# Optimization experiments

Measured on AMD Instinct MI355X. Metric: run time of the kernel, lower is better.

Reference implementation:

```python
import jax, jax.numpy as jnp
import numpy as np

B, L, SIZE, BACK, H = 4, 1024, 1024, 512, 16
D = SIZE // H  # head_size = 64


def setup_inputs() -> dict:
    key = jax.random.key(0)
    ks = jax.random.split(key, 18)
    s = 0.02
    return {
        "k": jax.random.normal(ks[0], (B, L, SIZE), jnp.float32),
        "v": jax.random.normal(ks[1], (B, L, SIZE), jnp.float32),
        "q": jax.random.normal(ks[2], (B, L, SIZE), jnp.float32),
        "background": jax.random.normal(ks[3], (B, L, BACK), jnp.float32),
        # weights stored [in, out] (pre-transposed vs torch Linear)
        "Wk": jax.random.normal(ks[4], (SIZE, SIZE), jnp.float32) * s,
        "bk": jnp.zeros((SIZE,), jnp.float32),
        "Wv": jax.random.normal(ks[5], (SIZE, SIZE), jnp.float32) * s,
        "bv": jnp.zeros((SIZE,), jnp.float32),
        "Wq": jax.random.normal(ks[6], (SIZE, SIZE), jnp.float32) * s,
        "bq": jnp.zeros((SIZE,), jnp.float32),
        "Wb": jax.random.normal(ks[7], (BACK, SIZE), jnp.float32) * s,
        "bb": jnp.zeros((SIZE,), jnp.float32),
        "Wo": jax.random.normal(ks[8], (SIZE, SIZE), jnp.float32) * s,
        "bo": jnp.zeros((SIZE,), jnp.float32),
    }


def _heads(x):
    # [B, L, H*D] -> [B, H, L, D]
    b, l, _ = x.shape
    return x.reshape(b, l, H, D).transpose(0, 2, 1, 3)


def reference(k, v, q, background, Wk, bk, Wv, bv, Wq, bq, Wb, bb, Wo, bo):
    kh = _heads(k @ Wk + bk)
    vh = _heads(v @ Wv + bv)
    qh = _heads(q @ Wq + bq) / jnp.sqrt(jnp.asarray(D, k.dtype))
    gh = _heads(background @ Wb + bb)
    scores = jnp.einsum("bhqd,bhkd->bhqk", qh, kh)   # [B,H,Lq,Lk]
    gates = jax.nn.sigmoid(jnp.einsum("bhqd,bhkd->bhqk", qh, gh))
    attn = jax.nn.softmax(scores, axis=-1) * gates    # dropout = identity (eval)
    ctx = jnp.einsum("bhqk,bhkd->bhqd", attn, vh)
    ctx = ctx.transpose(0, 2, 1, 3).reshape(k.shape[0], -1, H * D)
    return ctx @ Wo + bo
```

## Files before the change

kernel.cpp:

```cpp
#include <hip/hip_runtime.h>
#include <cstddef>
#include <cstdint>

typedef __attribute__((ext_vector_type(8))) short s16x8;
typedef __attribute__((ext_vector_type(4))) short s16x4;
typedef __attribute__((ext_vector_type(4))) float f32x4;

#define MFMA(a, b, c) __builtin_amdgcn_mfma_f32_16x16x32_bf16(a, b, c, 0, 0, 0)
#define LOG2E 1.44269504088896f

__device__ __forceinline__ short f2bf(float x) {
    uint32_t u = __float_as_uint(x);
    u = (u + 0x7FFFu + ((u >> 16) & 1u)) >> 16;
    return (short)u;
}

__device__ __forceinline__ void gld16(const void* g, void* l) {
    __builtin_amdgcn_global_load_lds(
        (const __attribute__((address_space(1))) unsigned int*)g,
        (__attribute__((address_space(3))) unsigned int*)l, 16, 0, 0);
}

__device__ __forceinline__ float fexp2(float x) {
#if __has_builtin(__builtin_amdgcn_exp2f)
    return __builtin_amdgcn_exp2f(x);
#else
    return exp2f(x);
#endif
}

__device__ __forceinline__ float frcp(float x) {
#if __has_builtin(__builtin_amdgcn_rcpf)
    return __builtin_amdgcn_rcpf(x);
#else
    return 1.f / x;
#endif
}

__device__ __forceinline__ unsigned cvtpk(float lo, float hi) {
    unsigned r;
    asm("v_cvt_pk_bf16_f32 %0, %1, %2" : "=v"(r) : "v"(lo), "v"(hi));
    return r;
}

struct ConvP { const float* in[4]; short* out[4]; };

__global__ __launch_bounds__(256)
void conv_all(ConvP p) {
    const int i = blockIdx.x * 256 + threadIdx.x;
    int r, base;
    if (i < 524288)            { r = 0; base = 0; }
    else if (i < 1048576)      { r = 1; base = 524288; }
    else if (i < 1310720)      { r = 2; base = 1048576; }
    else                       { r = 3; base = 1310720; }
    const int j = i - base;
    const float4 a = *(const float4*)(p.in[r] + (size_t)j * 8);
    const float4 b = *(const float4*)(p.in[r] + (size_t)j * 8 + 4);
    s16x8 o;
    o[0] = f2bf(a.x); o[1] = f2bf(a.y); o[2] = f2bf(a.z); o[3] = f2bf(a.w);
    o[4] = f2bf(b.x); o[5] = f2bf(b.y); o[6] = f2bf(b.z); o[7] = f2bf(b.w);
    *(s16x8*)(p.out[r] + (size_t)j * 8) = o;
}

struct WtP { const float* W[5]; short* Wt[5]; int K[5]; };

__global__ __launch_bounds__(256)
void conv_wt_b(WtP p) {
    __shared__ float T[64][65];
    const int z = blockIdx.z;
    const int K = p.K[z];
    const int k0 = blockIdx.y << 6, n0 = blockIdx.x << 6;
    if (k0 >= K) return;
    const float* W = p.W[z];
    short* Wt = p.Wt[z];
    const int tr = threadIdx.x >> 4, tc4 = (threadIdx.x & 15) << 2;
    #pragma unroll
    for (int i = 0; i < 4; ++i) {
        const int r = tr + i * 16;
        const float4 v = *(const float4*)(W + (size_t)(k0 + r) * 1024 + n0 + tc4);
        T[r][tc4 + 0] = v.x; T[r][tc4 + 1] = v.y;
        T[r][tc4 + 2] = v.z; T[r][tc4 + 3] = v.w;
    }
    __syncthreads();
    #pragma unroll
    for (int i = 0; i < 4; ++i) {
        const int nr = tr + i * 16;
        s16x4 o;
        o[0] = f2bf(T[tc4 + 0][nr]); o[1] = f2bf(T[tc4 + 1][nr]);
        o[2] = f2bf(T[tc4 + 2][nr]); o[3] = f2bf(T[tc4 + 3][nr]);
        *(s16x4*)(Wt + (size_t)(n0 + nr) * K + k0 + tc4) = o;
    }
}

struct Proj5P {
    const short* A[5]; const short* Bt[5]; const float* bias[5];
    void* Y[5]; int Kd[5]; float alpha[5]; int mode[5];
};

__global__ __launch_bounds__(256, 2)
void proj_gemm128d(Proj5P p, int zbase) {
    __shared__ __align__(16) short lds[2 * 16384];

    const int tid = threadIdx.x;
    const int w = tid >> 6, lane = tid & 63;
    const int la = lane & 15, kg = lane >> 4;
    const int wr = w >> 1, wc = w & 1;

    const int cpx = gridDim.x >> 3;
    const int orig = blockIdx.x;
    const int swz = (orig & 7) * cpx + (orig >> 3);
    const int z = zbase + (swz >> 8);
    const int rem = swz & 255;
    const int bm = rem >> 3, bn = rem & 7;

    const short* __restrict__ A  = p.A[z];
    const short* __restrict__ Bt = p.Bt[z];
    const int K = p.Kd[z];
    const int NT = K >> 6;

    const int srow = tid >> 3;
    const int csrc = (tid & 7) ^ (srow & 7);
    const short* gA = A  + (size_t)(bm * 128 + srow) * K + csrc * 8;
    const short* gB = Bt + (size_t)(bn * 128 + srow) * K + csrc * 8;
    short* dstA = &lds[srow * 64 + (tid & 7) * 8];
    short* dstB = dstA + 8192;

#define STAGE(t, nb) do {                                                  \
        const size_t ko_ = (size_t)((t) << 6);                             \
        short* ba_ = dstA + (nb) * 16384;                                  \
        short* bb_ = dstB + (nb) * 16384;                                  \
        _Pragma("unroll")                                                  \
        for (int i = 0; i < 4; ++i) {                                      \
            gld16(gA + (size_t)(32 * i) * K + ko_, ba_ + i * 2048);        \
            gld16(gB + (size_t)(32 * i) * K + ko_, bb_ + i * 2048);       \
        }                                                                  \
    } while (0)

    const int c0 = kg ^ (la & 7), c1 = (4 + kg) ^ (la & 7);
    const int aRd = (wr * 64 + la) * 64;
    const int bRd = 8192 + (wc * 64 + la) * 64;

    f32x4 acc[4][4] = {};

    STAGE(0, 0);
    asm volatile("s_waitcnt vmcnt(0)" ::: "memory");
    asm volatile("s_barrier" ::: "memory");

    for (int t = 0; t < NT; ++t) {
        const int cb = (t & 1) * 16384;
        if (t + 1 < NT) STAGE(t + 1, (t & 1) ^ 1);
        s16x8 af[4][2], bf[4][2];
        #pragma unroll
        for (int m = 0; m < 4; ++m) {
            af[m][0] = *(const s16x8*)&lds[cb + aRd + m * 1024 + c0 * 8];
            af[m][1] = *(const s16x8*)&lds[cb + aRd + m * 1024 + c1 * 8];
        }
        #pragma unroll
        for (int n = 0; n < 4; ++n) {
            bf[n][0] = *(const s16x8*)&lds[cb + bRd + n * 1024 + c0 * 8];
            bf[n][1] = *(const s16x8*)&lds[cb + bRd + n * 1024 + c1 * 8];
        }
        __builtin_amdgcn_s_setprio(1);
        #pragma unroll
        for (int m = 0; m < 4; ++m)
            #pragma unroll
            for (int n = 0; n < 4; ++n) {
                acc[m][n] = MFMA(af[m][0], bf[n][0], acc[m][n]);
                acc[m][n] = MFMA(af[m][1], bf[n][1], acc[m][n]);
            }
        __builtin_amdgcn_s_setprio(0);
        if (t + 1 < NT) {
            asm volatile("s_waitcnt vmcnt(0)" ::: "memory");
            asm volatile("s_barrier" ::: "memory");
        }
    }
#undef STAGE

    const float* __restrict__ bias = p.bias[z];
    const float alpha = p.alpha[z];
    const int mode = p.mode[z];

    if (mode == 2) {
        short* __restrict__ Y = (short*)p.Y[z];
        short* Tv = lds;
        asm volatile("s_waitcnt lgkmcnt(0)" ::: "memory");
        asm volatile("s_barrier" ::: "memory");
        #pragma unroll
        for (int ni = 0; ni < 4; ++ni) {
            const int rrow = wc * 64 + ni * 16 + la;
            const float bs = bias[bn * 128 + rrow];
            #pragma unroll
            for (int mi = 0; mi < 4; ++mi) {
                const int l0 = wr * 64 + mi * 16 + kg * 4;
                const unsigned d0 = cvtpk(alpha * (acc[mi][ni][0] + bs),
                                          alpha * (acc[mi][ni][1] + bs));
                const unsigned d1 = cvtpk(alpha * (acc[mi][ni][2] + bs),
                                          alpha * (acc[mi][ni][3] + bs));
                *(unsigned*)&Tv[rrow * 132 + l0]     = d0;
                *(unsigned*)&Tv[rrow * 132 + l0 + 2] = d1;
            }
        }
        asm volatile("s_barrier" ::: "memory");
        const int bb_ = (bm * 128) >> 10;
        const int l0g = (bm * 128) & 1023;
        #pragma unroll
        for (int s = 0; s < 8; ++s) {
            const int c = tid + (s << 8);
            const int rr = c >> 4, seg = c & 15;
            const int hh = bn * 2 + (rr >> 6), dd = rr & 63;
            const s16x8 vv = *(const s16x8*)&Tv[rr * 132 + seg * 8];
            *(s16x8*)&Y[((((size_t)bb_ * 16 + hh) * 64 + dd) << 10) + l0g + seg * 8] = vv;
        }
        return;
    }

    #pragma unroll
    for (int n = 0; n < 4; ++n) {
        const int col = bn * 128 + wc * 64 + n * 16 + la;
        const float bs = bias[col];
        #pragma unroll
        for (int m = 0; m < 4; ++m) {
            const int row0 = bm * 128 + wr * 64 + m * 16 + kg * 4;
            #pragma unroll
            for (int r = 0; r < 4; ++r) {
                const float v = alpha * (acc[m][n][r] + bs);
                if (mode == 0) {
                    ((short*)p.Y[z])[(size_t)(row0 + r) * 1024 + col] = f2bf(v);
                } else {
                    ((float*)p.Y[z])[(size_t)(row0 + r) * 1024 + col] = v;
                }
            }
        }
    }
}

__global__ __launch_bounds__(512)
void attn_mfma(const short* __restrict__ qh, const short* __restrict__ kh,
               const short* __restrict__ gh, const short* __restrict__ vt,
               short* __restrict__ ctx) {
    __shared__ __align__(16) short lds[33792];

    const int tid = threadIdx.x, w = tid >> 6, lane = tid & 63;
    const int la = lane & 15, kg = lane >> 4;

    const int orig = blockIdx.x;
    const int xcd = orig & 7, i = orig >> 3;
    const int bh = xcd * 8 + (i >> 3);
    const int qt = i & 7;
    const int b = bh >> 4, h = bh & 15;
    const int q0 = qt << 7;

    const size_t hb = ((size_t)b << 20) + ((size_t)h << 6);
    const size_t vtbase = ((size_t)bh) << 16;

    const int qrow = q0 + w * 16 + la;
    const s16x8 aq0 = *(const s16x8*)(qh + hb + (size_t)qrow * 1024 + kg * 8);
    const s16x8 aq1 = *(const s16x8*)(qh + hb + (size_t)qrow * 1024 + 32 + kg * 8);

    const int sr = tid >> 3, sc = tid & 7;
    const int cs = sc ^ (sr & 7);
    const short* ksrc = kh + hb + (size_t)sr * 1024 + cs * 8;
    const short* gsrc = gh + hb + (size_t)sr * 1024 + cs * 8;
    const short* vsrc = vt + vtbase + (size_t)sr * 1024 + cs * 8;
    const int sdst = tid * 8;

    const int ch0 = (kg ^ (la & 7)) * 8;
    const int ch1 = ((4 + kg) ^ (la & 7)) * 8;
    const int pbase = 24576 + w * 1152;

    float s_run = 0.f;
    f32x4 o[4] = {};

#define ASTG(kt, bb) do {                                                  \
        const size_t kr_ = (size_t)((kt) << 6) * 1024;                     \
        gld16(ksrc + kr_, &lds[(bb) * 4096 + sdst]);                       \
        gld16(gsrc + kr_, &lds[8192 + (bb) * 4096 + sdst]);                \
        gld16(vsrc + ((kt) << 6), &lds[16384 + (bb) * 4096 + sdst]);       \
    } while (0)

    ASTG(0, 0);
    asm volatile("s_waitcnt vmcnt(0)" ::: "memory");
    asm volatile("s_barrier" ::: "memory");

    for (int kt = 0; kt < 16; ++kt) {
        const int cb = (kt & 1) * 4096;
        if (kt < 15) ASTG(kt + 1, (kt + 1) & 1);

        f32x4 st[4] = {}, gt[4] = {};
        #pragma unroll
        for (int nf = 0; nf < 4; ++nf) {
            const int rb = cb + (nf * 16 + la) * 64;
            const s16x8 kb0 = *(const s16x8*)&lds[rb + ch0];
            const s16x8 kb1 = *(const s16x8*)&lds[rb + ch1];
            st[nf] = MFMA(kb0, aq0, st[nf]);
            st[nf] = MFMA(kb1, aq1, st[nf]);
            const s16x8 gb0 = *(const s16x8*)&lds[8192 + rb + ch0];
            const s16x8 gb1 = *(const s16x8*)&lds[8192 + rb + ch1];
            gt[nf] = MFMA(gb0, aq0, gt[nf]);
            gt[nf] = MFMA(gb1, aq1, gt[nf]);
        }

        float ps = 0.f;
        unsigned pkw[4][2];
        #pragma unroll
        for (int nf = 0; nf < 4; ++nf) {
            const float p0 = fexp2(st[nf][0]);
            const float p1 = fexp2(st[nf][1]);
            const float p2 = fexp2(st[nf][2]);
            const float p3 = fexp2(st[nf][3]);
            ps += (p0 + p1) + (p2 + p3);
            const float g0 = frcp(1.f + fexp2(-gt[nf][0]));
            const float g1 = frcp(1.f + fexp2(-gt[nf][1]));
            const float g2 = frcp(1.f + fexp2(-gt[nf][2]));
            const float g3 = frcp(1.f + fexp2(-gt[nf][3]));
            pkw[nf][0] = cvtpk(p0 * g0, p1 * g1);
            pkw[nf][1] = cvtpk(p2 * g2, p3 * g3);
        }
        s_run += ps;

        #pragma unroll
        for (int nf = 0; nf < 4; ++nf) {
            *(unsigned*)&lds[pbase + la * 72 + nf * 16 + kg * 4]     = pkw[nf][0];
            *(unsigned*)&lds[pbase + la * 72 + nf * 16 + kg * 4 + 2] = pkw[nf][1];
        }

        const s16x8 pa0 = *(const s16x8*)&lds[pbase + la * 72 + kg * 8];
        const s16x8 pa1 = *(const s16x8*)&lds[pbase + la * 72 + 32 + kg * 8];
        #pragma unroll
        for (int nf = 0; nf < 4; ++nf) {
            const int rb = cb + (nf * 16 + la) * 64;
            const s16x8 vb0 = *(const s16x8*)&lds[16384 + rb + ch0];
            const s16x8 vb1 = *(const s16x8*)&lds[16384 + rb + ch1];
            o[nf] = MFMA(vb0, pa0, o[nf]);
            o[nf] = MFMA(vb1, pa1, o[nf]);
        }

        if (kt < 15) {
            asm volatile("s_waitcnt vmcnt(0)" ::: "memory");
            asm volatile("s_barrier" ::: "memory");
        }
    }
#undef ASTG

    float sv = s_run;
    sv += __shfl_xor(sv, 16);
    sv += __shfl_xor(sv, 32);
    const float inv = frcp(sv);
    short* crow = ctx + ((size_t)(b * 1024 + qrow) << 10) + (h << 6);
    #pragma unroll
    for (int nf = 0; nf < 4; ++nf) {
        *(unsigned*)(crow + nf * 16 + kg * 4)     = cvtpk(o[nf][0] * inv, o[nf][1] * inv);
        *(unsigned*)(crow + nf * 16 + kg * 4 + 2) = cvtpk(o[nf][2] * inv, o[nf][3] * inv);
    }
}

extern "C" void kernel_launch(void* const* d_in, const int* in_sizes, int n_in,
                              void* d_out, int out_size, void* d_ws, size_t ws_size,
                              hipStream_t stream) {
    (void)in_sizes; (void)n_in; (void)out_size; (void)ws_size;

    const float* k  = (const float*)d_in[0];
    const float* v  = (const float*)d_in[1];
    const float* q  = (const float*)d_in[2];
    const float* bg = (const float*)d_in[3];
    const float* Wk = (const float*)d_in[4];  const float* bk = (const float*)d_in[5];
    const float* Wv = (const float*)d_in[6];  const float* bv = (const float*)d_in[7];
    const float* Wq = (const float*)d_in[8];  const float* bq = (const float*)d_in[9];
    const float* Wb = (const float*)d_in[10]; const float* bb = (const float*)d_in[11];
    const float* Wo = (const float*)d_in[12]; const float* bo = (const float*)d_in[13];

    short* ws = (short*)d_ws;
    const size_t MN = (size_t)4096 * 1024;
    short* khb = ws;
    short* qhb = ws + MN;
    short* ghb = ws + 2 * MN;
    short* vtb = ws + 3 * MN;
    short* xk  = ws + 4 * MN;
    short* xq  = ws + 5 * MN;
    short* xg  = ws + 6 * MN;
    short* xv  = ws + 6 * MN + MN / 2;
    short* wkt = ws + 7 * MN + MN / 2;
    short* wvt = wkt + 1048576;
    short* wqt = wvt + 1048576;
    short* wot = wqt + 1048576;
    short* wbt = wot + 1048576;
    short* ctxb = xk;

    const dim3 blk(256);

    WtP wp;
    wp.W[0] = Wk; wp.Wt[0] = wkt; wp.K[0] = 1024;
    wp.W[1] = Wv; wp.Wt[1] = wvt; wp.K[1] = 1024;
    wp.W[2] = Wq; wp.Wt[2] = wqt; wp.K[2] = 1024;
    wp.W[3] = Wb; wp.Wt[3] = wbt; wp.K[3] = 512;
    wp.W[4] = Wo; wp.Wt[4] = wot; wp.K[4] = 1024;
    conv_wt_b<<<dim3(16, 16, 5), blk, 0, stream>>>(wp);

    ConvP cp;
    cp.in[0] = k;  cp.out[0] = xk;
    cp.in[1] = q;  cp.out[1] = xq;
    cp.in[2] = bg; cp.out[2] = xg;
    cp.in[3] = v;  cp.out[3] = xv;
    conv_all<<<7168, blk, 0, stream>>>(cp);

    Proj5P p5;
    p5.A[0] = xk;   p5.Bt[0] = wkt; p5.bias[0] = bk; p5.Y[0] = khb;
    p5.Kd[0] = 1024; p5.alpha[0] = LOG2E;  p5.mode[0] = 0;
    p5.A[1] = xq;   p5.Bt[1] = wqt; p5.bias[1] = bq; p5.Y[1] = qhb;
    p5.Kd[1] = 1024; p5.alpha[1] = 0.125f; p5.mode[1] = 0;
    p5.A[2] = xg;   p5.Bt[2] = wbt; p5.bias[2] = bb; p5.Y[2] = ghb;
    p5.Kd[2] = 512;  p5.alpha[2] = LOG2E;  p5.mode[2] = 0;
    p5.A[3] = xv;   p5.Bt[3] = wvt; p5.bias[3] = bv; p5.Y[3] = vtb;
    p5.Kd[3] = 1024; p5.alpha[3] = 1.0f;   p5.mode[3] = 2;
    p5.A[4] = ctxb; p5.Bt[4] = wot; p5.bias[4] = bo; p5.Y[4] = d_out;
    p5.Kd[4] = 1024; p5.alpha[4] = 1.0f;   p5.mode[4] = 1;

    proj_gemm128d<<<dim3(1024), blk, 0, stream>>>(p5, 0);

    attn_mfma<<<dim3(512), dim3(512), 0, stream>>>(qhb, khb, ghb, vtb, ctxb);

    proj_gemm128d<<<dim3(256), blk, 0, stream>>>(p5, 4);
}
```

Before: 118.6 us.

## Use 256x256 ping-pong GEMM for QKVG projections and 128x64 tiles for output

The four input projections move to a new 512-thread kernel with 256x256 tiles. It splits each K-step into 32-wide halves, interleaves LDS reads, async global-to-LDS loads and MFMA phases across barriers, and launches exactly 256 blocks, one per CU. The output projection gets a dedicated kernel with 128x64 tiles and 512 blocks so that more blocks cover the CUs. Attention MFMA sections also get setprio hints. The larger tiles raise arithmetic intensity at the cost of a single block per CU and tighter barrier-driven scheduling.

```diff
diff --git a/kernel.cpp b/kernel.cpp
--- a/kernel.cpp
+++ b/kernel.cpp
@@ -92,71 +92,234 @@
     }
 }
 
-struct Proj5P {
-    const short* A[5]; const short* Bt[5]; const float* bias[5];
-    void* Y[5]; int Kd[5]; float alpha[5]; int mode[5];
+struct Proj4P {
+    const short* A[4]; const short* Bt[4]; const float* bias[4];
+    short* Y[4]; int Kd[4]; float alpha[4]; int mode[4];
 };
 
-__global__ __launch_bounds__(256, 2)
-void proj_gemm128d(Proj5P p, int zbase) {
-    __shared__ __align__(16) short lds[2 * 16384];
+__global__ __launch_bounds__(512, 1)
+void proj_gemm256p(Proj4P p) {
+    __shared__ __align__(16) short lds[65536];
+
+    const int tid = threadIdx.x;
+    const int w = tid >> 6, lane = tid & 63;
+    const int la = lane & 15, kg = lane >> 4;
+    const int wr = w >> 2, wc = w & 3;
+
+    const int orig = blockIdx.x;
+    const int swz = (orig & 7) * 32 + (orig >> 3);
+    const int z = swz >> 6;
+    const int rem = swz & 63;
+    const int bm = rem >> 2, bn = rem & 3;
+
+    const short* __restrict__ A  = p.A[z];
+    const short* __restrict__ Bt = p.Bt[z];
+    const int K = p.Kd[z];
+    const int NT = K >> 6;
+
+    const int sr = tid >> 2, sc = tid & 3;
+    const int csw = sc ^ ((sr >> 1) & 3);
+    const short* gA = A  + (size_t)(bm * 256 + sr) * K + csw * 8;
+    const short* gB = Bt + (size_t)(bn * 256 + sr) * K + csw * 8;
+    const int sdst = sr * 32 + sc * 8;
+
+#define STG_A(kt, buf, ks) do {                                            \
+        const size_t off_ = (size_t)((kt) * 64 + (ks) * 32);               \
+        short* d_ = &lds[(buf) * 16384 + (ks) * 8192 + sdst];              \
+        gld16(gA + off_, d_);                                              \
+        gld16(gA + (size_t)128 * K + off_, d_ + 4096);                     \
+    } while (0)
+#define STG_B(kt, buf, ks) do {                                            \
+        const size_t off_ = (size_t)((kt) * 64 + (ks) * 32);               \
+        short* d_ = &lds[32768 + (buf) * 16384 + (ks) * 8192 + sdst];      \
+        gld16(gB + off_, d_);                                              \
+        gld16(gB + (size_t)128 * K + off_, d_ + 4096);                     \
+    } while (0)
+
+    const int ach = (kg ^ ((la >> 1) & 3)) * 8;
+    const int aRow = (wr * 128 + la) * 32;
+    const int bRow = 32768 + (wc * 64 + la) * 32;
+
+    s16x8 af[4], bf[4];
+    f32x4 acc[8][4] = {};
+
+#define LDA(buf, mh, ks) do { _Pragma("unroll")                            \
+    for (int mf = 0; mf < 4; ++mf)                                         \
+        af[mf] = *(const s16x8*)&lds[(buf) * 16384 + (ks) * 8192 + aRow    \
+                                     + (mh) * 2048 + mf * 512 + ach];      \
+    } while (0)
+#define LDB(buf, ks) do { _Pragma("unroll")                                \
+    for (int nf = 0; nf < 4; ++nf)                                         \
+        bf[nf] = *(const s16x8*)&lds[(buf) * 16384 + (ks) * 8192 + bRow    \
+                                     + nf * 512 + ach];                    \
+    } while (0)
+#define MF(mh) do { __builtin_amdgcn_s_setprio(1); _Pragma("unroll")       \
+    for (int mf = 0; mf < 4; ++mf) _Pragma("unroll")                       \
+    for (int nf = 0; nf < 4; ++nf)                                         \
+        acc[(mh) * 4 + mf][nf] = MFMA(af[mf], bf[nf], acc[(mh) * 4 + mf][nf]); \
+    __builtin_amdgcn_s_setprio(0); } while (0)
+#define BARR() __builtin_amdgcn_s_barrier()
+#define LGKM0() do { asm volatile("s_waitcnt lgkmcnt(0)" ::: "memory");    \
+                     __builtin_amdgcn_sched_barrier(0); } while (0)
+#define VMW(n) asm volatile("s_waitcnt vmcnt(" #n ")" ::: "memory")
+
+    STG_A(0, 0, 0); STG_B(0, 0, 0);
+    STG_A(0, 0, 1); STG_B(0, 0, 1);
+    STG_A(1, 1, 0); STG_B(1, 1, 0);
+    VMW(8);
+    BARR();
+
+    for (int t = 0; t < NT; ++t) {
+        const int buf = t & 1, nbuf = buf ^ 1;
+        LDA(buf, 0, 0); LDB(buf, 0);
+        if (t + 1 < NT) STG_A(t + 1, nbuf, 1);
+        BARR(); LGKM0(); MF(0);
+        BARR();
+        LDA(buf, 1, 0);
+        if (t + 1 < NT) STG_B(t + 1, nbuf, 1);
+        BARR(); LGKM0(); MF(1);
+        if (t + 1 < NT) { VMW(6); } else { VMW(0); }
+        BARR();
+        LDA(buf, 1, 1); LDB(buf, 1);
+        if (t + 2 < NT) STG_A(t + 2, buf, 0);
+        BARR(); LGKM0(); MF(1);
+        BARR();
+        LDA(buf, 0, 1);
+        if (t + 2 < NT) STG_B(t + 2, buf, 0);
+        BARR(); LGKM0(); MF(0);
+        if (t + 2 < NT) { VMW(6); } else if (t + 1 < NT) { VMW(2); }
+        BARR();
+    }
+#undef STG_A
+#undef STG_B
+#undef LDA
+#undef LDB
+#undef MF
+
+    const float* __restrict__ bias = p.bias[z];
+    const float alpha = p.alpha[z];
+
+    if (p.mode[z] == 0) {
+        short* __restrict__ Y = p.Y[z];
+        #pragma unroll
+        for (int nf = 0; nf < 4; ++nf) {
+            const int col = bn * 256 + wc * 64 + nf * 16 + la;
+            const float bs = bias[col];
+            #pragma unroll
+            for (int g = 0; g < 8; ++g) {
+                const int row0 = bm * 256 + wr * 128 + (g >> 2) * 64 + (g & 3) * 16 + kg * 4;
+                #pragma unroll
+                for (int r = 0; r < 4; ++r)
+                    Y[(size_t)(row0 + r) * 1024 + col] = f2bf(alpha * (acc[g][nf][r] + bs));
+            }
+        }
+        return;
+    }
+
+    {
+        short* __restrict__ Y = p.Y[z];
+        const int bb_ = (bm * 256) >> 10;
+        const int l0g = (bm * 256) & 1023;
+        #pragma unroll
+        for (int ph = 0; ph < 2; ++ph) {
+            BARR();
+            if ((wc >> 1) == ph) {
+                #pragma unroll
+                for (int nf = 0; nf < 4; ++nf) {
+                    const int col = wc * 64 + nf * 16 + la;
+                    const int cp = col - ph * 128;
+                    const float bs = bias[bn * 256 + col];
+                    #pragma unroll
+                    for (int g = 0; g < 8; ++g) {
+                        const int row = wr * 128 + (g >> 2) * 64 + (g & 3) * 16 + kg * 4;
+                        const unsigned d0 = cvtpk(alpha * (acc[g][nf][0] + bs),
+                                                  alpha * (acc[g][nf][1] + bs));
+                        const unsigned d1 = cvtpk(alpha * (acc[g][nf][2] + bs),
+                                                  alpha * (acc[g][nf][3] + bs));
+                        *(unsigned*)&lds[cp * 264 + row]     = d0;
+                        *(unsigned*)&lds[cp * 264 + row + 2] = d1;
+                    }
+                }
+            }
+            asm volatile("s_waitcnt lgkmcnt(0)" ::: "memory");
+            BARR();
+            const int cp = tid >> 2;
+            const int colg = bn * 256 + ph * 128 + cp;
+            const int hh = colg >> 6, dd = colg & 63;
+            const size_t ybase = ((((size_t)bb_ * 16 + hh) * 64 + dd) << 10) + l0g;
+            #pragma unroll
+            for (int s = 0; s < 8; ++s) {
+                const int rchunk = (tid & 3) + s * 4;
+                *(s16x8*)&Y[ybase + rchunk * 8] =
+                    *(const s16x8*)&lds[cp * 264 + rchunk * 8];
+            }
+            BARR();
+        }
+    }
+#undef BARR
+#undef LGKM0
+#undef VMW
+}
+
+struct ProjOP {
+    const short* A; const short* Bt; const float* bias; float* Y;
+};
+
+__global__ __launch_bounds__(256, 3)
+void proj_gemmO(ProjOP p) {
+    __shared__ __align__(16) short lds[2 * 12288];
 
     const int tid = threadIdx.x;
     const int w = tid >> 6, lane = tid & 63;
     const int la = lane & 15, kg = lane >> 4;
     const int wr = w >> 1, wc = w & 1;
 
-    const int cpx = gridDim.x >> 3;
     const int orig = blockIdx.x;
-    const int swz = (orig & 7) * cpx + (orig >> 3);
-    const int z = zbase + (swz >> 8);
-    const int rem = swz & 255;
-    const int bm = rem >> 3, bn = rem & 7;
-
-    const short* __restrict__ A  = p.A[z];
-    const short* __restrict__ Bt = p.Bt[z];
-    const int K = p.Kd[z];
-    const int NT = K >> 6;
+    const int swz = (orig & 7) * 64 + (orig >> 3);
+    const int bm = swz >> 4, bn = swz & 15;
+
+    const int K = 1024, NT = 16;
 
     const int srow = tid >> 3;
     const int csrc = (tid & 7) ^ (srow & 7);
-    const short* gA = A  + (size_t)(bm * 128 + srow) * K + csrc * 8;
-    const short* gB = Bt + (size_t)(bn * 128 + srow) * K + csrc * 8;
+    const short* gA = p.A  + (size_t)(bm * 128 + srow) * K + csrc * 8;
+    const short* gB = p.Bt + (size_t)(bn * 64 + srow) * K + csrc * 8;
     short* dstA = &lds[srow * 64 + (tid & 7) * 8];
     short* dstB = dstA + 8192;
 
 #define STAGE(t, nb) do {                                                  \
         const size_t ko_ = (size_t)((t) << 6);                             \
-        short* ba_ = dstA + (nb) * 16384;                                  \
-        short* bb_ = dstB + (nb) * 16384;                                  \
         _Pragma("unroll")                                                  \
-        for (int i = 0; i < 4; ++i) {                                      \
-            gld16(gA + (size_t)(32 * i) * K + ko_, ba_ + i * 2048);        \
-            gld16(gB + (size_t)(32 * i) * K + ko_, bb_ + i * 2048);       \
-        }                                                                  \
+        for (int i = 0; i < 4; ++i)                                        \
+            gld16(gA + (size_t)(32 * i) * K + ko_,                         \
+                  dstA + (nb) * 12288 + i * 2048);                         \
+        _Pragma("unroll")                                                  \
+        for (int i = 0; i < 2; ++i)                                        \
+            gld16(gB + (size_t)(32 * i) * K + ko_,                         \
+                  dstB + (nb) * 12288 + i * 2048);                         \
     } while (0)
 
     const int c0 = kg ^ (la & 7), c1 = (4 + kg) ^ (la & 7);
     const int aRd = (wr * 64 + la) * 64;
-    const int bRd = 8192 + (wc * 64 + la) * 64;
-
-    f32x4 acc[4][4] = {};
+    const int bRd = 8192 + (wc * 32 + la) * 64;
+
+    f32x4 acc[4][2] = {};
 
     STAGE(0, 0);
     asm volatile("s_waitcnt vmcnt(0)" ::: "memory");
     asm volatile("s_barrier" ::: "memory");
 
     for (int t = 0; t < NT; ++t) {
-        const int cb = (t & 1) * 16384;
+        const int cb = (t & 1) * 12288;
         if (t + 1 < NT) STAGE(t + 1, (t & 1) ^ 1);
-        s16x8 af[4][2], bf[4][2];
+        s16x8 af[4][2], bf[2][2];
         #pragma unroll
         for (int m = 0; m < 4; ++m) {
             af[m][0] = *(const s16x8*)&lds[cb + aRd + m * 1024 + c0 * 8];
             af[m][1] = *(const s16x8*)&lds[cb + aRd + m * 1024 + c1 * 8];
         }
         #pragma unroll
-        for (int n = 0; n < 4; ++n) {
+        for (int n = 0; n < 2; ++n) {
             bf[n][0] = *(const s16x8*)&lds[cb + bRd + n * 1024 + c0 * 8];
             bf[n][1] = *(const s16x8*)&lds[cb + bRd + n * 1024 + c1 * 8];
         }
@@ -164,7 +327,7 @@
         #pragma unroll
         for (int m = 0; m < 4; ++m)
             #pragma unroll
-            for (int n = 0; n < 4; ++n) {
+            for (int n = 0; n < 2; ++n) {
                 acc[m][n] = MFMA(af[m][0], bf[n][0], acc[m][n]);
                 acc[m][n] = MFMA(af[m][1], bf[n][1], acc[m][n]);
             }
@@ -176,60 +339,16 @@
     }
 #undef STAGE
 
-    const float* __restrict__ bias = p.bias[z];
-    const float alpha = p.alpha[z];
-    const int mode = p.mode[z];
-
-    if (mode == 2) {
-        short* __restrict__ Y = (short*)p.Y[z];
-        short* Tv = lds;
-        asm volatile("s_waitcnt lgkmcnt(0)" ::: "memory");
-        asm volatile("s_barrier" ::: "memory");
-        #pragma unroll
-        for (int ni = 0; ni < 4; ++ni) {
-            const int rrow = wc * 64 + ni * 16 + la;
-            const float bs = bias[bn * 128 + rrow];
-            #pragma unroll
-            for (int mi = 0; mi < 4; ++mi) {
-                const int l0 = wr * 64 + mi * 16 + kg * 4;
-                const unsigned d0 = cvtpk(alpha * (acc[mi][ni][0] + bs),
-                                          alpha * (acc[mi][ni][1] + bs));
-                const unsigned d1 = cvtpk(alpha * (acc[mi][ni][2] + bs),
-                                          alpha * (acc[mi][ni][3] + bs));
-                *(unsigned*)&Tv[rrow * 132 + l0]     = d0;
-                *(unsigned*)&Tv[rrow * 132 + l0 + 2] = d1;
-            }
-        }
-        asm volatile("s_barrier" ::: "memory");
-        const int bb_ = (bm * 128) >> 10;
-        const int l0g = (bm * 128) & 1023;
-        #pragma unroll
-        for (int s = 0; s < 8; ++s) {
-            const int c = tid + (s << 8);
-            const int rr = c >> 4, seg = c & 15;
-            const int hh = bn * 2 + (rr >> 6), dd = rr & 63;
-            const s16x8 vv = *(const s16x8*)&Tv[rr * 132 + seg * 8];
-            *(s16x8*)&Y[((((size_t)bb_ * 16 + hh) * 64 + dd) << 10) + l0g + seg * 8] = vv;
-        }
-        return;
-    }
-
     #pragma unroll
-    for (int n = 0; n < 4; ++n) {
-        const int col = bn * 128 + wc * 64 + n * 16 + la;
-        const float bs = bias[col];
+    for (int n = 0; n < 2; ++n) {
+        const int col = bn * 64 + wc * 32 + n * 16 + la;
+        const float bs = p.bias[col];
         #pragma unroll
         for (int m = 0; m < 4; ++m) {
             const int row0 = bm * 128 + wr * 64 + m * 16 + kg * 4;
             #pragma unroll
-            for (int r = 0; r < 4; ++r) {
-                const float v = alpha * (acc[m][n][r] + bs);
-                if (mode == 0) {
-                    ((short*)p.Y[z])[(size_t)(row0 + r) * 1024 + col] = f2bf(v);
-                } else {
-                    ((float*)p.Y[z])[(size_t)(row0 + r) * 1024 + col] = v;
-                }
-            }
+            for (int r = 0; r < 4; ++r)
+                p.Y[(size_t)(row0 + r) * 1024 + col] = acc[m][n][r] + bs;
         }
     }
 }
@@ -287,6 +406,7 @@
         if (kt < 15) ASTG(kt + 1, (kt + 1) & 1);
 
         f32x4 st[4] = {}, gt[4] = {};
+        __builtin_amdgcn_s_setprio(1);
         #pragma unroll
         for (int nf = 0; nf < 4; ++nf) {
             const int rb = cb + (nf * 16 + la) * 64;
@@ -299,6 +419,7 @@
             gt[nf] = MFMA(gb0, aq0, gt[nf]);
             gt[nf] = MFMA(gb1, aq1, gt[nf]);
         }
+        __builtin_amdgcn_s_setprio(0);
 
         float ps = 0.f;
         unsigned pkw[4][2];
@@ -326,6 +447,7 @@
 
         const s16x8 pa0 = *(const s16x8*)&lds[pbase + la * 72 + kg * 8];
         const s16x8 pa1 = *(const s16x8*)&lds[pbase + la * 72 + 32 + kg * 8];
+        __builtin_amdgcn_s_setprio(1);
         #pragma unroll
         for (int nf = 0; nf < 4; ++nf) {
             const int rb = cb + (nf * 16 + la) * 64;
@@ -334,6 +456,7 @@
             o[nf] = MFMA(vb0, pa0, o[nf]);
             o[nf] = MFMA(vb1, pa1, o[nf]);
         }
+        __builtin_amdgcn_s_setprio(0);
 
         if (kt < 15) {
             asm volatile("s_waitcnt vmcnt(0)" ::: "memory");
@@ -403,21 +526,20 @@
     cp.in[3] = v;  cp.out[3] = xv;
     conv_all<<<7168, blk, 0, stream>>>(cp);
 
-    Proj5P p5;
-    p5.A[0] = xk;   p5.Bt[0] = wkt; p5.bias[0] = bk; p5.Y[0] = khb;
-    p5.Kd[0] = 1024; p5.alpha[0] = LOG2E;  p5.mode[0] = 0;
-    p5.A[1] = xq;   p5.Bt[1] = wqt; p5.bias[1] = bq; p5.Y[1] = qhb;
-    p5.Kd[1] = 1024; p5.alpha[1] = 0.125f; p5.mode[1] = 0;
-    p5.A[2] = xg;   p5.Bt[2] = wbt; p5.bias[2] = bb; p5.Y[2] = ghb;
-    p5.Kd[2] = 512;  p5.alpha[2] = LOG2E;  p5.mode[2] = 0;
-    p5.A[3] = xv;   p5.Bt[3] = wvt; p5.bias[3] = bv; p5.Y[3] = vtb;
-    p5.Kd[3] = 1024; p5.alpha[3] = 1.0f;   p5.mode[3] = 2;
-    p5.A[4] = ctxb; p5.Bt[4] = wot; p5.bias[4] = bo; p5.Y[4] = d_out;
-    p5.Kd[4] = 1024; p5.alpha[4] = 1.0f;   p5.mode[4] = 1;
-
-    proj_gemm128d<<<dim3(1024), blk, 0, stream>>>(p5, 0);
+    Proj4P p4;
+    p4.A[0] = xk; p4.Bt[0] = wkt; p4.bias[0] = bk; p4.Y[0] = khb;
+    p4.Kd[0] = 1024; p4.alpha[0] = LOG2E;  p4.mode[0] = 0;
+    p4.A[1] = xq; p4.Bt[1] = wqt; p4.bias[1] = bq; p4.Y[1] = qhb;
+    p4.Kd[1] = 1024; p4.alpha[1] = 0.125f; p4.mode[1] = 0;
+    p4.A[2] = xg; p4.Bt[2] = wbt; p4.bias[2] = bb; p4.Y[2] = ghb;
+    p4.Kd[2] = 512;  p4.alpha[2] = LOG2E;  p4.mode[2] = 0;
+    p4.A[3] = xv; p4.Bt[3] = wvt; p4.bias[3] = bv; p4.Y[3] = vtb;
+    p4.Kd[3] = 1024; p4.alpha[3] = 1.0f;   p4.mode[3] = 2;
+    proj_gemm256p<<<dim3(256), dim3(512), 0, stream>>>(p4);
 
     attn_mfma<<<dim3(512), dim3(512), 0, stream>>>(qhb, khb, ghb, vtb, ctxb);
 
-    proj_gemm128d<<<dim3(256), blk, 0, stream>>>(p5, 4);
-}
+    ProjOP po;
+    po.A = ctxb; po.Bt = wot; po.bias = bo; po.Y = (float*)d_out;
+    proj_gemmO<<<dim3(512), blk, 0, stream>>>(po);
+}
```

Result: no change. 117.7 us (-0.7%).
